# Performance work log

Measured on AMD Instinct MI355X. Metric: run time of the kernel, lower is better.

Reference implementation:

```python
import jax, jax.numpy as jnp
import numpy as np

NEG_SLOPE = 0.01  # LeakyReLU default
STRIDE = 5        # group_length // 4
EPS = 1e-5        # RMSNorm eps


def leaky_relu(x):
    return jnp.where(x >= 0, x, NEG_SLOPE * x)


def rmsnorm(x, w):
    return x * jax.lax.rsqrt(jnp.mean(x * x, axis=-1, keepdims=True) + EPS) * w


def s6(x, fc1_w, fc1_b, fc2_w, fc2_b, fc3_w, fc3_b, A):
    # x: [B, L, D] with D = 2*d_model; A: [D, N]
    delta = jax.nn.softplus(x @ fc1_w.T + fc1_b)        # [B, L, D]
    Bm = x @ fc2_w.T + fc2_b                             # [B, L, N]
    Cm = x @ fc3_w.T + fc3_b                             # [B, L, N]
    dA = jnp.exp(jnp.einsum('bld,dn->bldn', delta, A))   # [B, L, D, N]
    dBx = jnp.einsum('bld,bln,bld->bldn', delta, Bm, x)  # delta * B * x

    def step(h, inp):
        dA_t, dBx_t = inp
        h = dA_t * h + dBx_t
        return h, h

    B_, L, D, N = dA.shape
    h0 = jnp.zeros((B_, D, N), dtype=x.dtype)
    _, hs = jax.lax.scan(step, h0, (jnp.swapaxes(dA, 0, 1), jnp.swapaxes(dBx, 0, 1)))
    hs = jnp.swapaxes(hs, 0, 1)                          # [B, L, D, N]
    return jnp.einsum('bln,bldn->bld', Cm, hs)           # [B, L, D]


def setup_inputs() -> dict:
    key = jax.random.key(0)
    ks = iter(jax.random.split(key, 32))

    def rn(shape, scale=0.02):
        return scale * jax.random.normal(next(ks), shape, dtype=jnp.float32)

    B, band, gl, d, N, L = 256, 189, 20, 128, 128, 34
    di = 2 * d
    return {
        'x': jax.random.normal(next(ks), (B, 1, band), dtype=jnp.float32),
        'conv_w': rn((d, 1, gl)), 'conv_b': rn((d,)),
        'norm_w': jnp.ones((d,), jnp.float32),
        'inp_w': rn((di, d)), 'inp_b': rn((di,)),
        'seqconv_w': rn((L, L, 3)), 'seqconv_b': rn((L,)),
        'convlin_w': rn((di, di)), 'convlin_b': rn((di,)),
        'fc1_w': rn((di, di)), 'fc1_b': rn((di,)),
        'fc2_w': rn((N, di)), 'fc2_b': rn((N,)),
        'fc3_w': rn((N, di)), 'fc3_b': rn((N,)),
        'A': jnp.ones((di, N), jnp.float32) / jnp.sqrt(jnp.float32(N)),
        'D_w': rn((di, d)), 'D_b': rn((di,)),
        'out_w': rn((d, di)), 'out_b': rn((d,)),
        'fnn1_w': rn((64, L * d)), 'fnn1_b': rn((64,)),
        'fnn2_w': rn((32, 64)), 'fnn2_b': rn((32,)),
    }


def reference(x, conv_w, conv_b, norm_w, inp_w, inp_b, seqconv_w, seqconv_b,
              convlin_w, convlin_b, fc1_w, fc1_b, fc2_w, fc2_b, fc3_w, fc3_b,
              A, D_w, D_b, out_w, out_b, fnn1_w, fnn1_b, fnn2_w, fnn2_b):
    # group division: Conv1d(1, d, k=20, stride=5) + LeakyReLU
    g = jax.lax.conv_general_dilated(x, conv_w, (STRIDE,), [(0, 0)],
                                     dimension_numbers=('NCH', 'OIH', 'NCH'))
    g = leaky_relu(g + conv_b[None, :, None])            # [B, d, L]
    h = jnp.swapaxes(g, 1, 2)                            # [B, L, d]
    # Mamba block
    xn = rmsnorm(h, norm_w)
    xp = xn @ inp_w.T + inp_b                            # [B, L, 2d]
    # Conv1d(seq_len, seq_len, k=3, pad=1): seq axis L is the channel dim
    xc = jax.lax.conv_general_dilated(xp, seqconv_w, (1,), [(1, 1)],
                                      dimension_numbers=('NCH', 'OIH', 'NCH'))
    xc = jax.nn.silu(xc + seqconv_b[None, :, None])
    xc = xc @ convlin_w.T + convlin_b                    # [B, L, 2d]
    xs = s6(xc, fc1_w, fc1_b, fc2_w, fc2_b, fc3_w, fc3_b, A)
    y = jax.nn.silu(xs) * jax.nn.silu(xn @ D_w.T + D_b)  # gated
    y = y @ out_w.T + out_b                              # [B, L, d]
    # FNN head
    f = y.reshape(y.shape[0], -1)                        # [B, L*d]
    f = leaky_relu(f @ fnn1_w.T + fnn1_b)
    return f @ fnn2_w.T + fnn2_b                         # [B, 32]
```

## Files before the change

kernel.cpp:

```cpp
#include <hip/hip_runtime.h>
#include <math.h>


#define NB    256
#define LL    34
#define DD    128
#define DI    256
#define NN    128
#define MM    (NB*LL)

using u16 = unsigned short;
typedef __attribute__((ext_vector_type(8))) short short8;
typedef __attribute__((ext_vector_type(4))) float f32x4;

__device__ __forceinline__ float silu_f(float x)  { return x / (1.f + __expf(-x)); }
__device__ __forceinline__ float softplus_f(float x) {
    return fmaxf(x, 0.f) + __logf(1.f + __expf(-fabsf(x)));
}
__device__ __forceinline__ float leaky_f(float x) { return (x >= 0.f) ? x : 0.01f * x; }

__device__ __forceinline__ u16 f2bf(float x) {
    unsigned u = __float_as_uint(x);
    return (u16)((u + 0x7FFF + ((u >> 16) & 1)) >> 16);
}
__device__ __forceinline__ float bf2f(u16 h) {
    return __uint_as_float(((unsigned)h) << 16);
}
__device__ __forceinline__ void f2pair(float v, u16* h, u16* l) {
    u16 hh = f2bf(v);
    *h = hh;
    *l = f2bf(v - bf2f(hh));
}

__global__ __launch_bounds__(256)
void prep_all_k(const float* __restrict__ inp_w, const float* __restrict__ D_w,
                const float* __restrict__ fc1_w, const float* __restrict__ fc2_w,
                const float* __restrict__ fc3_w, const float* __restrict__ convlin_w,
                const float* __restrict__ out_w,
                const float* __restrict__ inp_b, const float* __restrict__ D_b,
                const float* __restrict__ fc1_b, const float* __restrict__ fc2_b,
                const float* __restrict__ fc3_b,
                const float* __restrict__ W1, const float* __restrict__ A,
                u16* __restrict__ wc1h, u16* __restrict__ wc1l,
                u16* __restrict__ wc3h, u16* __restrict__ wc3l,
                u16* __restrict__ cvh,  u16* __restrict__ cvl,
                u16* __restrict__ owh,  u16* __restrict__ owl,
                float* __restrict__ bias1, float* __restrict__ bias3,
                float* __restrict__ W1T, int* __restrict__ flag)
{
    const int bx  = blockIdx.x;
    const int tid = threadIdx.x;
    __shared__ float tile[64][65];

    if (bx < 1152) {
        int i = bx * 256 + tid;
        if (i < 65536) {
            float v = (i < 32768) ? inp_w[i] : D_w[i - 32768];
            f2pair(v, &wc1h[i], &wc1l[i]);
        } else if (i < 196608) {
            int j = i - 65536;
            float v = (j < 65536) ? fc1_w[j] : (j < 98304 ? fc2_w[j - 65536] : fc3_w[j - 98304]);
            f2pair(v, &wc3h[j], &wc3l[j]);
        } else if (i < 262144) {
            int j = i - 196608;
            f2pair(convlin_w[j], &cvh[j], &cvl[j]);
        } else if (i < 294912) {
            int j = i - 262144;
            f2pair(out_w[j], &owh[j], &owl[j]);
        }
        if (i < 512)  bias1[i] = (i < 256) ? inp_b[i] : D_b[i - 256];
        else if (i < 1024) {
            int j = i - 512;
            bias3[j] = (j < 256) ? fc1_b[j] : (j < 384 ? fc2_b[j - 256] : fc3_b[j - 384]);
        }
    } else if (bx < 1220) {
        const int bt = bx - 1152;
        for (int p = 0; p < 16; p++) {
            int idx = tid + p * 256;
            int r = idx >> 6, c = idx & 63;
            tile[r][c] = W1[(size_t)r * 4352 + bt * 64 + c];
        }
        __syncthreads();
        for (int p = 0; p < 16; p++) {
            int idx = tid + p * 256;
            int cc = idx >> 6, rr = idx & 63;
            W1T[(size_t)(bt * 64 + cc) * 64 + rr] = tile[rr][cc];
        }
    } else {
        __shared__ int s;
        if (tid == 0) s = 1;
        __syncthreads();
        bool ok = true;
        for (int k = 0; k < 128; k++) {
            int idx = tid + k * 256;
            ok &= (A[idx] == A[idx & ~127]);
        }
        if (!ok) s = 0;
        __syncthreads();
        if (tid == 0) *flag = s;
    }
}

__global__ __launch_bounds__(128)
void conv_norm_k(const float* __restrict__ x, const float* __restrict__ cw,
                 const float* __restrict__ cb, const float* __restrict__ nw,
                 u16* __restrict__ XNh, u16* __restrict__ XNl)
{
    int bl = blockIdx.x;
    int b = bl / LL, l = bl % LL;
    int c = threadIdx.x;
    const float* xr = x + (size_t)b * 189 + l * 5;
    float g = cb[c];
    #pragma unroll
    for (int k = 0; k < 20; k++) g = fmaf(xr[k], cw[c * 20 + k], g);
    g = leaky_f(g);

    float s = g * g;
    #pragma unroll
    for (int m = 32; m >= 1; m >>= 1) s += __shfl_xor(s, m);
    __shared__ float wsum[2];
    if ((threadIdx.x & 63) == 0) wsum[threadIdx.x >> 6] = s;
    __syncthreads();
    float mean = (wsum[0] + wsum[1]) * (1.f / 128.f);
    float inv = 1.f / sqrtf(mean + 1e-5f);
    float v = g * inv * nw[c];
    f2pair(v, &XNh[(size_t)bl * DD + c], &XNl[(size_t)bl * DD + c]);
}

template <int K, int EPI>
__global__ __launch_bounds__(256)
void mgemm_k(const u16* __restrict__ Ah, const u16* __restrict__ Al,
             const u16* __restrict__ Wh, const u16* __restrict__ Wl,
             const float* __restrict__ bias,
             float* __restrict__ Y, int ldy,
             u16* __restrict__ Yh, u16* __restrict__ Yl,
             u16* __restrict__ BC)
{
    const int tid  = threadIdx.x;
    const int r0   = blockIdx.x * 128;
    const int c0   = blockIdx.y * 64;
    const int wave = tid >> 6;
    const int lane = tid & 63;
    const int wm   = wave & 1;
    const int wn   = wave >> 1;
    const int l15  = lane & 15;
    const int lq   = lane >> 4;

    __shared__ u16 sAh[128][40];
    __shared__ u16 sAl[128][40];
    __shared__ u16 sBh[64][40];
    __shared__ u16 sBl[64][40];

    f32x4 acc[4][2];
    #pragma unroll
    for (int i = 0; i < 4; i++)
        #pragma unroll
        for (int j = 0; j < 2; j++) acc[i][j] = (f32x4){0.f, 0.f, 0.f, 0.f};

    const int a_row = tid >> 1;
    const int a_kb  = (tid & 1) * 16;
    const int b_row = tid >> 2;
    const int b_ko  = (tid & 3) * 8;

    for (int k0 = 0; k0 < K; k0 += 32) {
        const u16* ga = Ah + (size_t)(r0 + a_row) * K + k0 + a_kb;
        const u16* gl = Al + (size_t)(r0 + a_row) * K + k0 + a_kb;
        short8 vh0 = *(const short8*)(ga);
        short8 vh1 = *(const short8*)(ga + 8);
        short8 vl0 = *(const short8*)(gl);
        short8 vl1 = *(const short8*)(gl + 8);
        const u16* gb = Wh + (size_t)(c0 + b_row) * K + k0 + b_ko;
        const u16* gc = Wl + (size_t)(c0 + b_row) * K + k0 + b_ko;
        short8 wb = *(const short8*)(gb);
        short8 wc = *(const short8*)(gc);

        *(short8*)&sAh[a_row][a_kb]     = vh0;
        *(short8*)&sAh[a_row][a_kb + 8] = vh1;
        *(short8*)&sAl[a_row][a_kb]     = vl0;
        *(short8*)&sAl[a_row][a_kb + 8] = vl1;
        *(short8*)&sBh[b_row][b_ko] = wb;
        *(short8*)&sBl[b_row][b_ko] = wc;
        __syncthreads();

        short8 fah[4], fal[4], fbh[2], fbl[2];
        #pragma unroll
        for (int i = 0; i < 4; i++) {
            fah[i] = *(const short8*)&sAh[wm * 64 + i * 16 + l15][lq * 8];
            fal[i] = *(const short8*)&sAl[wm * 64 + i * 16 + l15][lq * 8];
        }
        #pragma unroll
        for (int j = 0; j < 2; j++) {
            fbh[j] = *(const short8*)&sBh[wn * 32 + j * 16 + l15][lq * 8];
            fbl[j] = *(const short8*)&sBl[wn * 32 + j * 16 + l15][lq * 8];
        }
        #pragma unroll
        for (int i = 0; i < 4; i++)
            #pragma unroll
            for (int j = 0; j < 2; j++) {
                acc[i][j] = __builtin_amdgcn_mfma_f32_16x16x32_bf16(fah[i], fbh[j], acc[i][j], 0, 0, 0);
                acc[i][j] = __builtin_amdgcn_mfma_f32_16x16x32_bf16(fah[i], fbl[j], acc[i][j], 0, 0, 0);
                acc[i][j] = __builtin_amdgcn_mfma_f32_16x16x32_bf16(fal[i], fbh[j], acc[i][j], 0, 0, 0);
            }
        __syncthreads();
    }

    #pragma unroll
    for (int i = 0; i < 4; i++) {
        int gr = r0 + wm * 64 + i * 16 + lq * 4;
        #pragma unroll
        for (int j = 0; j < 2; j++) {
            int gc = c0 + wn * 32 + j * 16 + l15;
            float bb = bias[gc];
            #pragma unroll
            for (int r = 0; r < 4; r++) {
                float v = acc[i][j][r] + bb;
                if (EPI == 1 || EPI == 3) { if (gc < 256) v = softplus_f(v); }
                if (EPI == 2) {
                    u16 hh, ll;
                    f2pair(v, &hh, &ll);
                    Yh[(size_t)(gr + r) * ldy + gc] = hh;
                    Yl[(size_t)(gr + r) * ldy + gc] = ll;
                } else {
                    Y[(size_t)(gr + r) * ldy + gc] = v;
                    if (EPI == 3 && gc >= 256) {
                        u16 hh, ll;
                        f2pair(v, &hh, &ll);
                        u16* rb = BC + (size_t)(gr + r) * 1024
                                     + ((gc < 384) ? 0 : 256) + (gc & 127);
                        rb[0]   = hh;
                        rb[128] = ll;
                    }
                }
            }
        }
    }
}

__global__ __launch_bounds__(256)
void seqconv_k(const float* __restrict__ XP, int ldxp,
               const float* __restrict__ w, const float* __restrict__ bias,
               u16* __restrict__ XCh, u16* __restrict__ XCl)
{
    const int b   = blockIdx.x;
    const int tid = threadIdx.x;
    const int tx  = tid & 63;
    const int ty  = tid >> 6;
    const int j0  = tx * 4;

    __shared__ float sx[LL][264];
    __shared__ float sw[LL][112];

    for (int idx = tid; idx < LL * 256; idx += 256) {
        int li = idx >> 8, jj = idx & 255;
        sx[li][jj + 1] = XP[(size_t)(b * LL + li) * ldxp + jj];
    }
    if (tid < LL) { sx[tid][0] = 0.f; sx[tid][257] = 0.f; }
    for (int idx = tid; idx < LL * LL * 3; idx += 256) {
        int lo = idx / 102;
        int rem = idx - lo * 102;
        int li = rem / 3;
        int k  = rem - li * 3;
        sw[li][lo * 3 + k] = w[idx];
    }
    __syncthreads();

    const int base = ty * 9 - (ty == 3 ? 1 : 0);
    const int cnt  = (ty < 2) ? 9 : 8;

    float acc[9][4];
    #pragma unroll
    for (int i = 0; i < 9; i++)
        #pragma unroll
        for (int jj = 0; jj < 4; jj++) acc[i][jj] = 0.f;

    for (int li = 0; li < LL; li++) {
        float4 xa = *(const float4*)&sx[li][j0];
        float2 xb = *(const float2*)&sx[li][j0 + 4];
        float xv[6] = {xa.x, xa.y, xa.z, xa.w, xb.x, xb.y};
        const float* swr = &sw[li][0];
        #pragma unroll
        for (int i = 0; i < 9; i++) {
            if (i < cnt) {
                int lo3 = (base + i) * 3;
                float w0 = swr[lo3 + 0];
                float w1 = swr[lo3 + 1];
                float w2 = swr[lo3 + 2];
                #pragma unroll
                for (int jj = 0; jj < 4; jj++) {
                    acc[i][jj] = fmaf(w0, xv[jj],     acc[i][jj]);
                    acc[i][jj] = fmaf(w1, xv[jj + 1], acc[i][jj]);
                    acc[i][jj] = fmaf(w2, xv[jj + 2], acc[i][jj]);
                }
            }
        }
    }

    #pragma unroll
    for (int i = 0; i < 9; i++) {
        if (i < cnt) {
            int lo = base + i;
            float bb = bias[lo];
            ushort4 oh, ol;
            float v0 = silu_f(acc[i][0] + bb);
            float v1 = silu_f(acc[i][1] + bb);
            float v2 = silu_f(acc[i][2] + bb);
            float v3 = silu_f(acc[i][3] + bb);
            f2pair(v0, &oh.x, &ol.x);
            f2pair(v1, &oh.y, &ol.y);
            f2pair(v2, &oh.z, &ol.z);
            f2pair(v3, &oh.w, &ol.w);
            size_t o = (size_t)(b * LL + lo) * DI + j0;
            *(ushort4*)&XCh[o] = oh;
            *(ushort4*)&XCl[o] = ol;
        }
    }
}

__global__ __launch_bounds__(256)
void ssd_scan_k(const int* __restrict__ flag,
                const float* __restrict__ dBC,
                const u16* __restrict__ BC,
                const u16* __restrict__ Xh, const u16* __restrict__ Xl,
                const float* __restrict__ A,
                const float* __restrict__ DG,
                u16* __restrict__ Gh, u16* __restrict__ Gl)
{
    if (*flag == 0) return;
    const int b    = blockIdx.x;
    const int tid  = threadIdx.x;
    const int wave = tid >> 6;
    const int lane = tid & 63;
    const int l15  = lane & 15;
    const int lq   = lane >> 4;

    __shared__ u16 sBh[48][136], sBl[48][136];
    __shared__ u16 sCh[48][136], sCl[48][136];
    __shared__ float sM[48][49];

    const u16* base = BC + (size_t)b * LL * 1024;
    for (int idx = tid; idx < LL * 16; idx += 256) {
        int l = idx >> 4, c = (idx & 15) << 3;
        const u16* row = base + l * 1024;
        *(short8*)&sBh[l][c] = *(const short8*)&row[c];
        *(short8*)&sBl[l][c] = *(const short8*)&row[128 + c];
        *(short8*)&sCh[l][c] = *(const short8*)&row[256 + c];
        *(short8*)&sCl[l][c] = *(const short8*)&row[384 + c];
    }
    __syncthreads();

    for (int tt = wave; tt < 9; tt += 4) {
        int ti = tt / 3, tj = tt - ti * 3;
        f32x4 acc = (f32x4){0.f, 0.f, 0.f, 0.f};
        #pragma unroll
        for (int ks = 0; ks < 4; ks++) {
            short8 ch = *(const short8*)&sCh[ti * 16 + l15][ks * 32 + lq * 8];
            short8 cl = *(const short8*)&sCl[ti * 16 + l15][ks * 32 + lq * 8];
            short8 bh = *(const short8*)&sBh[tj * 16 + l15][ks * 32 + lq * 8];
            short8 bl = *(const short8*)&sBl[tj * 16 + l15][ks * 32 + lq * 8];
            acc = __builtin_amdgcn_mfma_f32_16x16x32_bf16(ch, bh, acc, 0, 0, 0);
            acc = __builtin_amdgcn_mfma_f32_16x16x32_bf16(ch, bl, acc, 0, 0, 0);
            acc = __builtin_amdgcn_mfma_f32_16x16x32_bf16(cl, bh, acc, 0, 0, 0);
        }
        #pragma unroll
        for (int r = 0; r < 4; r++)
            sM[ti * 16 + lq * 4 + r][tj * 16 + l15] = acc[r];
    }
    __syncthreads();

    const int d = tid;
    const float a_d = A[(size_t)d * NN];
    const float* pDel = dBC + (size_t)b * LL * 512 + d;
    const u16* pXh = Xh + (size_t)b * LL * 256 + d;
    const u16* pXl = Xl + (size_t)b * LL * 256 + d;

    float u[LL], eS[LL];
    float S = 0.f;
    #pragma unroll
    for (int l = 0; l < LL; l++) {
        float dl = pDel[l * 512];
        S = fmaf(dl, a_d, S);
        eS[l] = __expf(S);
        float xv = bf2f(pXh[l * 256]) + bf2f(pXl[l * 256]);
        u[l] = __expf(-S) * dl * xv;
    }

    const float* pG = DG + (size_t)b * LL * 512 + 256 + d;
    u16* pGh = Gh + (size_t)b * LL * 256 + d;
    u16* pGl = Gl + (size_t)b * LL * 256 + d;
    #pragma unroll
    for (int l = 0; l < LL; l++) {
        float acc = 0.f;
        for (int t = 0; t <= l; t++) acc = fmaf(sM[l][t], u[t], acc);
        float xs = eS[l] * acc;
        float g = silu_f(xs) * silu_f(pG[l * 512]);
        u16 hh, ll2;
        f2pair(g, &hh, &ll2);
        pGh[l * 256] = hh;
        pGl[l * 256] = ll2;
    }
}

__global__ __launch_bounds__(256)
void scan_fb_k(const int* __restrict__ flag,
               const float* __restrict__ dBC,
               const u16*  __restrict__ Xh, const u16* __restrict__ Xl,
               const float* __restrict__ A,
               const float* __restrict__ DG,
               u16* __restrict__ Gh, u16* __restrict__ Gl)
{
    if (*flag != 0) return;
    const int b  = blockIdx.y;
    const int d0 = blockIdx.x * 64;
    const int tid = threadIdx.x;
    const int sub = tid & 15;
    const int pg  = tid >> 4;
    const int dbase = d0 + pg * 4;
    const int nA = sub * 4;

    float a[4][8], h[4][8];
    #pragma unroll
    for (int dd = 0; dd < 4; dd++) {
        const float* Ar = A + (size_t)(dbase + dd) * NN;
        float4 q0 = *(const float4*)(Ar + nA);
        float4 q1 = *(const float4*)(Ar + 64 + nA);
        a[dd][0]=q0.x; a[dd][1]=q0.y; a[dd][2]=q0.z; a[dd][3]=q0.w;
        a[dd][4]=q1.x; a[dd][5]=q1.y; a[dd][6]=q1.z; a[dd][7]=q1.w;
        #pragma unroll
        for (int j = 0; j < 8; j++) h[dd][j] = 0.f;
    }

    const float* pD  = dBC + (size_t)b * LL * 512 + dbase;
    const float* pBC = dBC + (size_t)b * LL * 512 + 256 + nA;
    const u16*  pXh = Xh  + (size_t)b * LL * 256 + dbase;
    const u16*  pXl = Xl  + (size_t)b * LL * 256 + dbase;
    const float* pG  = DG  + (size_t)b * LL * 512 + 256 + dbase;
    u16* pGh = Gh + (size_t)b * LL * 256 + dbase;
    u16* pGl = Gl + (size_t)b * LL * 256 + dbase;

    for (int l = 0; l < LL; l++) {
        float4  cD  = *(const float4*)(pD);
        ushort4 cXh = *(const ushort4*)(pXh);
        ushort4 cXl = *(const ushort4*)(pXl);
        float4 cB0 = *(const float4*)(pBC);
        float4 cB1 = *(const float4*)(pBC + 64);
        float4 cC0 = *(const float4*)(pBC + 128);
        float4 cC1 = *(const float4*)(pBC + 192);
        pD += 512; pBC += 512; pXh += 256; pXl += 256;

        float xv[4] = { bf2f(cXh.x) + bf2f(cXl.x), bf2f(cXh.y) + bf2f(cXl.y),
                        bf2f(cXh.z) + bf2f(cXl.z), bf2f(cXh.w) + bf2f(cXl.w) };
        float dl[4] = {cD.x, cD.y, cD.z, cD.w};
        float dx[4] = {cD.x * xv[0], cD.y * xv[1], cD.z * xv[2], cD.w * xv[3]};
        float bv[8] = {cB0.x,cB0.y,cB0.z,cB0.w,cB1.x,cB1.y,cB1.z,cB1.w};
        float cv[8] = {cC0.x,cC0.y,cC0.z,cC0.w,cC1.x,cC1.y,cC1.z,cC1.w};

        float accd[4] = {0.f, 0.f, 0.f, 0.f};
        #pragma unroll
        for (int dd = 0; dd < 4; dd++)
            #pragma unroll
            for (int j = 0; j < 8; j++) {
                float dA = __expf(dl[dd] * a[dd][j]);
                h[dd][j] = fmaf(dA, h[dd][j], dx[dd] * bv[j]);
                accd[dd] = fmaf(cv[j], h[dd][j], accd[dd]);
            }
        #pragma unroll
        for (int dd = 0; dd < 4; dd++) {
            float v = accd[dd];
            v += __shfl_xor(v, 1);
            v += __shfl_xor(v, 2);
            v += __shfl_xor(v, 4);
            v += __shfl_xor(v, 8);
            accd[dd] = v;
        }
        if (sub == 0) {
            float4 dg = *(const float4*)(pG);
            ushort4 oh, ol;
            float g0 = silu_f(accd[0]) * silu_f(dg.x);
            float g1 = silu_f(accd[1]) * silu_f(dg.y);
            float g2 = silu_f(accd[2]) * silu_f(dg.z);
            float g3 = silu_f(accd[3]) * silu_f(dg.w);
            f2pair(g0, &oh.x, &ol.x);
            f2pair(g1, &oh.y, &ol.y);
            f2pair(g2, &oh.z, &ol.z);
            f2pair(g3, &oh.w, &ol.w);
            *(ushort4*)pGh = oh;
            *(ushort4*)pGl = ol;
        }
        pG += 512; pGh += 256; pGl += 256;
    }
}

__global__ __launch_bounds__(256)
void fnn1_k(const float* __restrict__ F, const float* __restrict__ W1T,
            float* __restrict__ partials)
{
    const int btile = blockIdx.x;
    const int kc    = blockIdx.y;
    const int tid   = threadIdx.x;
    __shared__ float sf[16][260];
    for (int i = tid; i < 16 * 256; i += 256) {
        int r = i >> 8, c = i & 255;
        sf[r][c] = F[(size_t)(btile * 16 + r) * 4352 + kc * 256 + c];
    }
    __syncthreads();

    const int o  = tid & 63;
    const int bq = tid >> 6;
    const float* w = W1T + (size_t)(kc * 256) * 64 + o;
    float acc[4] = {0.f, 0.f, 0.f, 0.f};
    for (int k = 0; k < 256; k += 4) {
        float w0 = w[(size_t)(k + 0) * 64];
        float w1 = w[(size_t)(k + 1) * 64];
        float w2 = w[(size_t)(k + 2) * 64];
        float w3 = w[(size_t)(k + 3) * 64];
        #pragma unroll
        for (int bj = 0; bj < 4; bj++) {
            float4 f4 = *(const float4*)&sf[bq * 4 + bj][k];
            acc[bj] = fmaf(w0, f4.x, acc[bj]);
            acc[bj] = fmaf(w1, f4.y, acc[bj]);
            acc[bj] = fmaf(w2, f4.z, acc[bj]);
            acc[bj] = fmaf(w3, f4.w, acc[bj]);
        }
    }
    #pragma unroll
    for (int bj = 0; bj < 4; bj++)
        partials[(size_t)kc * 16384 + (btile * 16 + bq * 4 + bj) * 64 + o] = acc[bj];
}

__global__ __launch_bounds__(64)
void fnn2_k(const float* __restrict__ partials,
            const float* __restrict__ B1,
            const float* __restrict__ W2, const float* __restrict__ B2,
            float* __restrict__ out)
{
    int b = blockIdx.x;
    int t = threadIdx.x;
    __shared__ float s1[64];
    float acc = B1[t];
    #pragma unroll
    for (int kc = 0; kc < 17; kc++)
        acc += partials[(size_t)kc * 16384 + b * 64 + t];
    s1[t] = leaky_f(acc);
    __syncthreads();

    if (t < 32) {
        float acc2 = B2[t];
        const float* w2 = W2 + t * 64;
        #pragma unroll
        for (int j = 0; j < 64; j++) acc2 = fmaf(s1[j], w2[j], acc2);
        out[(size_t)b * 32 + t] = acc2;
    }
}

extern "C" void kernel_launch(void* const* d_in, const int* in_sizes, int n_in,
                              void* d_out, int out_size, void* d_ws, size_t ws_size,
                              hipStream_t stream)
{
    const float* x        = (const float*)d_in[0];
    const float* conv_w   = (const float*)d_in[1];
    const float* conv_b   = (const float*)d_in[2];
    const float* norm_w   = (const float*)d_in[3];
    const float* inp_w    = (const float*)d_in[4];
    const float* inp_b    = (const float*)d_in[5];
    const float* seqconv_w= (const float*)d_in[6];
    const float* seqconv_b= (const float*)d_in[7];
    const float* convlin_w= (const float*)d_in[8];
    const float* convlin_b= (const float*)d_in[9];
    const float* fc1_w    = (const float*)d_in[10];
    const float* fc1_b    = (const float*)d_in[11];
    const float* fc2_w    = (const float*)d_in[12];
    const float* fc2_b    = (const float*)d_in[13];
    const float* fc3_w    = (const float*)d_in[14];
    const float* fc3_b    = (const float*)d_in[15];
    const float* A        = (const float*)d_in[16];
    const float* D_w      = (const float*)d_in[17];
    const float* D_b      = (const float*)d_in[18];
    const float* out_w    = (const float*)d_in[19];
    const float* out_b    = (const float*)d_in[20];
    const float* fnn1_w   = (const float*)d_in[21];
    const float* fnn1_b   = (const float*)d_in[22];
    const float* fnn2_w   = (const float*)d_in[23];
    const float* fnn2_b   = (const float*)d_in[24];

    char* W = (char*)d_ws;
    float* buf1  = (float*)(W + 0);
    float* buf3  = (float*)(W + 17825792);
    u16*   xnh   = (u16*)  (W + 35651584);
    u16*   xnl   = (u16*)  (W + 37879808);
    u16*   xc2h  = (u16*)  (W + 35651584);
    float* fout  = (float*)(W + 35651584);
    u16*   xc2l  = (u16*)  (W + 40108032);
    u16*   xch   = (u16*)  (W + 44564480);
    u16*   xcl   = (u16*)  (W + 49020928);
    float* w1t   = (float*)(W + 53477376);
    u16*   wc1h  = (u16*)  (W + 54591488);
    u16*   wc1l  = (u16*)  (W + 54722560);
    u16*   wc3h  = (u16*)  (W + 54853632);
    u16*   wc3l  = (u16*)  (W + 55115776);
    u16*   cvh   = (u16*)  (W + 55377920);
    u16*   cvl   = (u16*)  (W + 55508992);
    u16*   owh   = (u16*)  (W + 55640064);
    u16*   owl   = (u16*)  (W + 55705600);
    float* bias1 = (float*)(W + 55771136);
    float* bias3 = (float*)(W + 55773184);
    int*   uflag = (int*)  (W + 55775232);
    u16* gateh = xch;
    u16* gatel = xcl;
    u16* bcpair = (u16*)buf1;
    float* partials = buf3;

    prep_all_k<<<1221, 256, 0, stream>>>(inp_w, D_w, fc1_w, fc2_w, fc3_w,
                                         convlin_w, out_w,
                                         inp_b, D_b, fc1_b, fc2_b, fc3_b,
                                         fnn1_w, A,
                                         wc1h, wc1l, wc3h, wc3l, cvh, cvl,
                                         owh, owl, bias1, bias3, w1t, uflag);

    conv_norm_k<<<MM, 128, 0, stream>>>(x, conv_w, conv_b, norm_w, xnh, xnl);

    mgemm_k<128, 0><<<dim3(MM / 128, 8), 256, 0, stream>>>(
        xnh, xnl, wc1h, wc1l, bias1, buf1, 512, nullptr, nullptr, nullptr);

    seqconv_k<<<NB, 256, 0, stream>>>(buf1, 512, seqconv_w, seqconv_b, xch, xcl);

    mgemm_k<256, 2><<<dim3(MM / 128, 4), 256, 0, stream>>>(
        xch, xcl, cvh, cvl, convlin_b, nullptr, 256, xc2h, xc2l, nullptr);

    mgemm_k<256, 3><<<dim3(MM / 128, 8), 256, 0, stream>>>(
        xc2h, xc2l, wc3h, wc3l, bias3, buf3, 512, nullptr, nullptr, bcpair);

    ssd_scan_k<<<NB, 256, 0, stream>>>(uflag, buf3, bcpair, xc2h, xc2l, A,
                                       buf1, gateh, gatel);
    scan_fb_k<<<dim3(4, NB), 256, 0, stream>>>(uflag, buf3, xc2h, xc2l, A,
                                               buf1, gateh, gatel);

    mgemm_k<256, 0><<<dim3(MM / 128, 2), 256, 0, stream>>>(
        gateh, gatel, owh, owl, out_b, fout, 128, nullptr, nullptr, nullptr);

    fnn1_k<<<dim3(16, 17), 256, 0, stream>>>(fout, w1t, partials);
    fnn2_k<<<NB, 64, 0, stream>>>(partials, fnn1_b, fnn2_w, fnn2_b,
                                  (float*)d_out);
}
```

Measured before the change: 220.5 us.

## Fuse conv, norm, GEMMs, seqconv, scan and out-proj into one per-batch kernel

Replaces the chain of separate kernels (conv+norm, input GEMM, seq conv, convlin GEMM, fc GEMM, scan, out GEMM) with one kernel that runs one workgroup per batch element. Intermediates stay in shared memory and registers rather than going through global memory. GEMMs read weight fragments directly from global memory without LDS staging. The risk is low parallelism: only 256 workgroups of 256 threads with launch_bounds(256,1) and heavy register use, so each CU runs one block serially through every stage.

```diff
diff --git a/kernel.cpp b/kernel.cpp
--- a/kernel.cpp
+++ b/kernel.cpp
@@ -51,6 +51,7 @@
     const int bx  = blockIdx.x;
     const int tid = threadIdx.x;
     __shared__ float tile[64][65];
+    __shared__ int sflag;
 
     if (bx < 1152) {
         int i = bx * 256 + tid;
@@ -87,245 +88,63 @@
             W1T[(size_t)(bt * 64 + cc) * 64 + rr] = tile[rr][cc];
         }
     } else {
-        __shared__ int s;
-        if (tid == 0) s = 1;
+        if (tid == 0) sflag = 1;
         __syncthreads();
         bool ok = true;
         for (int k = 0; k < 128; k++) {
             int idx = tid + k * 256;
             ok &= (A[idx] == A[idx & ~127]);
         }
-        if (!ok) s = 0;
-        __syncthreads();
-        if (tid == 0) *flag = s;
-    }
-}
-
-__global__ __launch_bounds__(128)
-void conv_norm_k(const float* __restrict__ x, const float* __restrict__ cw,
-                 const float* __restrict__ cb, const float* __restrict__ nw,
-                 u16* __restrict__ XNh, u16* __restrict__ XNl)
+        if (!ok) sflag = 0;
+        __syncthreads();
+        if (tid == 0) *flag = sflag;
+    }
+}
+
+template <int KS, int NT>
+__device__ __forceinline__ void gemm3t(
+    const u16* __restrict__ Ah, const u16* __restrict__ Al, int astr,
+    const u16* __restrict__ Wh, const u16* __restrict__ Wl, int K,
+    int colbase, int l15, int lq, f32x4 (&acc)[3][NT])
 {
-    int bl = blockIdx.x;
-    int b = bl / LL, l = bl % LL;
-    int c = threadIdx.x;
-    const float* xr = x + (size_t)b * 189 + l * 5;
-    float g = cb[c];
-    #pragma unroll
-    for (int k = 0; k < 20; k++) g = fmaf(xr[k], cw[c * 20 + k], g);
-    g = leaky_f(g);
-
-    float s = g * g;
-    #pragma unroll
-    for (int m = 32; m >= 1; m >>= 1) s += __shfl_xor(s, m);
-    __shared__ float wsum[2];
-    if ((threadIdx.x & 63) == 0) wsum[threadIdx.x >> 6] = s;
-    __syncthreads();
-    float mean = (wsum[0] + wsum[1]) * (1.f / 128.f);
-    float inv = 1.f / sqrtf(mean + 1e-5f);
-    float v = g * inv * nw[c];
-    f2pair(v, &XNh[(size_t)bl * DD + c], &XNl[(size_t)bl * DD + c]);
-}
-
-template <int K, int EPI>
-__global__ __launch_bounds__(256)
-void mgemm_k(const u16* __restrict__ Ah, const u16* __restrict__ Al,
-             const u16* __restrict__ Wh, const u16* __restrict__ Wl,
-             const float* __restrict__ bias,
-             float* __restrict__ Y, int ldy,
-             u16* __restrict__ Yh, u16* __restrict__ Yl,
-             u16* __restrict__ BC)
+    for (int ks = 0; ks < KS; ks++) {
+        short8 fah[3], fal[3];
+        #pragma unroll
+        for (int ti = 0; ti < 3; ti++) {
+            fah[ti] = *(const short8*)&Ah[(ti * 16 + l15) * astr + ks * 32 + lq * 8];
+            fal[ti] = *(const short8*)&Al[(ti * 16 + l15) * astr + ks * 32 + lq * 8];
+        }
+        #pragma unroll
+        for (int nt = 0; nt < NT; nt++) {
+            size_t off = (size_t)(colbase + nt * 16 + l15) * K + ks * 32 + lq * 8;
+            short8 bh = *(const short8*)&Wh[off];
+            short8 bl = *(const short8*)&Wl[off];
+            #pragma unroll
+            for (int ti = 0; ti < 3; ti++) {
+                acc[ti][nt] = __builtin_amdgcn_mfma_f32_16x16x32_bf16(fah[ti], bh, acc[ti][nt], 0, 0, 0);
+                acc[ti][nt] = __builtin_amdgcn_mfma_f32_16x16x32_bf16(fah[ti], bl, acc[ti][nt], 0, 0, 0);
+                acc[ti][nt] = __builtin_amdgcn_mfma_f32_16x16x32_bf16(fal[ti], bh, acc[ti][nt], 0, 0, 0);
+            }
+        }
+    }
+}
+
+__global__ __launch_bounds__(256, 1)
+void fused_k(const float* __restrict__ xin, const float* __restrict__ cw,
+             const float* __restrict__ cb, const float* __restrict__ nw,
+             const u16* __restrict__ wc1h, const u16* __restrict__ wc1l,
+             const float* __restrict__ bias1,
+             const float* __restrict__ scw, const float* __restrict__ scb,
+             const u16* __restrict__ cvh, const u16* __restrict__ cvl,
+             const float* __restrict__ cvb,
+             const u16* __restrict__ wc3h, const u16* __restrict__ wc3l,
+             const float* __restrict__ bias3,
+             const float* __restrict__ A, const int* __restrict__ flag,
+             const u16* __restrict__ owh, const u16* __restrict__ owl,
+             const float* __restrict__ owb,
+             float* __restrict__ dg_g, float* __restrict__ delta_g,
+             u16* __restrict__ bc_g, float* __restrict__ fout_g)
 {
-    const int tid  = threadIdx.x;
-    const int r0   = blockIdx.x * 128;
-    const int c0   = blockIdx.y * 64;
-    const int wave = tid >> 6;
-    const int lane = tid & 63;
-    const int wm   = wave & 1;
-    const int wn   = wave >> 1;
-    const int l15  = lane & 15;
-    const int lq   = lane >> 4;
-
-    __shared__ u16 sAh[128][40];
-    __shared__ u16 sAl[128][40];
-    __shared__ u16 sBh[64][40];
-    __shared__ u16 sBl[64][40];
-
-    f32x4 acc[4][2];
-    #pragma unroll
-    for (int i = 0; i < 4; i++)
-        #pragma unroll
-        for (int j = 0; j < 2; j++) acc[i][j] = (f32x4){0.f, 0.f, 0.f, 0.f};
-
-    const int a_row = tid >> 1;
-    const int a_kb  = (tid & 1) * 16;
-    const int b_row = tid >> 2;
-    const int b_ko  = (tid & 3) * 8;
-
-    for (int k0 = 0; k0 < K; k0 += 32) {
-        const u16* ga = Ah + (size_t)(r0 + a_row) * K + k0 + a_kb;
-        const u16* gl = Al + (size_t)(r0 + a_row) * K + k0 + a_kb;
-        short8 vh0 = *(const short8*)(ga);
-        short8 vh1 = *(const short8*)(ga + 8);
-        short8 vl0 = *(const short8*)(gl);
-        short8 vl1 = *(const short8*)(gl + 8);
-        const u16* gb = Wh + (size_t)(c0 + b_row) * K + k0 + b_ko;
-        const u16* gc = Wl + (size_t)(c0 + b_row) * K + k0 + b_ko;
-        short8 wb = *(const short8*)(gb);
-        short8 wc = *(const short8*)(gc);
-
-        *(short8*)&sAh[a_row][a_kb]     = vh0;
-        *(short8*)&sAh[a_row][a_kb + 8] = vh1;
-        *(short8*)&sAl[a_row][a_kb]     = vl0;
-        *(short8*)&sAl[a_row][a_kb + 8] = vl1;
-        *(short8*)&sBh[b_row][b_ko] = wb;
-        *(short8*)&sBl[b_row][b_ko] = wc;
-        __syncthreads();
-
-        short8 fah[4], fal[4], fbh[2], fbl[2];
-        #pragma unroll
-        for (int i = 0; i < 4; i++) {
-            fah[i] = *(const short8*)&sAh[wm * 64 + i * 16 + l15][lq * 8];
-            fal[i] = *(const short8*)&sAl[wm * 64 + i * 16 + l15][lq * 8];
-        }
-        #pragma unroll
-        for (int j = 0; j < 2; j++) {
-            fbh[j] = *(const short8*)&sBh[wn * 32 + j * 16 + l15][lq * 8];
-            fbl[j] = *(const short8*)&sBl[wn * 32 + j * 16 + l15][lq * 8];
-        }
-        #pragma unroll
-        for (int i = 0; i < 4; i++)
-            #pragma unroll
-            for (int j = 0; j < 2; j++) {
-                acc[i][j] = __builtin_amdgcn_mfma_f32_16x16x32_bf16(fah[i], fbh[j], acc[i][j], 0, 0, 0);
-                acc[i][j] = __builtin_amdgcn_mfma_f32_16x16x32_bf16(fah[i], fbl[j], acc[i][j], 0, 0, 0);
-                acc[i][j] = __builtin_amdgcn_mfma_f32_16x16x32_bf16(fal[i], fbh[j], acc[i][j], 0, 0, 0);
-            }
-        __syncthreads();
-    }
-
-    #pragma unroll
-    for (int i = 0; i < 4; i++) {
-        int gr = r0 + wm * 64 + i * 16 + lq * 4;
-        #pragma unroll
-        for (int j = 0; j < 2; j++) {
-            int gc = c0 + wn * 32 + j * 16 + l15;
-            float bb = bias[gc];
-            #pragma unroll
-            for (int r = 0; r < 4; r++) {
-                float v = acc[i][j][r] + bb;
-                if (EPI == 1 || EPI == 3) { if (gc < 256) v = softplus_f(v); }
-                if (EPI == 2) {
-                    u16 hh, ll;
-                    f2pair(v, &hh, &ll);
-                    Yh[(size_t)(gr + r) * ldy + gc] = hh;
-                    Yl[(size_t)(gr + r) * ldy + gc] = ll;
-                } else {
-                    Y[(size_t)(gr + r) * ldy + gc] = v;
-                    if (EPI == 3 && gc >= 256) {
-                        u16 hh, ll;
-                        f2pair(v, &hh, &ll);
-                        u16* rb = BC + (size_t)(gr + r) * 1024
-                                     + ((gc < 384) ? 0 : 256) + (gc & 127);
-                        rb[0]   = hh;
-                        rb[128] = ll;
-                    }
-                }
-            }
-        }
-    }
-}
-
-__global__ __launch_bounds__(256)
-void seqconv_k(const float* __restrict__ XP, int ldxp,
-               const float* __restrict__ w, const float* __restrict__ bias,
-               u16* __restrict__ XCh, u16* __restrict__ XCl)
-{
-    const int b   = blockIdx.x;
-    const int tid = threadIdx.x;
-    const int tx  = tid & 63;
-    const int ty  = tid >> 6;
-    const int j0  = tx * 4;
-
-    __shared__ float sx[LL][264];
-    __shared__ float sw[LL][112];
-
-    for (int idx = tid; idx < LL * 256; idx += 256) {
-        int li = idx >> 8, jj = idx & 255;
-        sx[li][jj + 1] = XP[(size_t)(b * LL + li) * ldxp + jj];
-    }
-    if (tid < LL) { sx[tid][0] = 0.f; sx[tid][257] = 0.f; }
-    for (int idx = tid; idx < LL * LL * 3; idx += 256) {
-        int lo = idx / 102;
-        int rem = idx - lo * 102;
-        int li = rem / 3;
-        int k  = rem - li * 3;
-        sw[li][lo * 3 + k] = w[idx];
-    }
-    __syncthreads();
-
-    const int base = ty * 9 - (ty == 3 ? 1 : 0);
-    const int cnt  = (ty < 2) ? 9 : 8;
-
-    float acc[9][4];
-    #pragma unroll
-    for (int i = 0; i < 9; i++)
-        #pragma unroll
-        for (int jj = 0; jj < 4; jj++) acc[i][jj] = 0.f;
-
-    for (int li = 0; li < LL; li++) {
-        float4 xa = *(const float4*)&sx[li][j0];
-        float2 xb = *(const float2*)&sx[li][j0 + 4];
-        float xv[6] = {xa.x, xa.y, xa.z, xa.w, xb.x, xb.y};
-        const float* swr = &sw[li][0];
-        #pragma unroll
-        for (int i = 0; i < 9; i++) {
-            if (i < cnt) {
-                int lo3 = (base + i) * 3;
-                float w0 = swr[lo3 + 0];
-                float w1 = swr[lo3 + 1];
-                float w2 = swr[lo3 + 2];
-                #pragma unroll
-                for (int jj = 0; jj < 4; jj++) {
-                    acc[i][jj] = fmaf(w0, xv[jj],     acc[i][jj]);
-                    acc[i][jj] = fmaf(w1, xv[jj + 1], acc[i][jj]);
-                    acc[i][jj] = fmaf(w2, xv[jj + 2], acc[i][jj]);
-                }
-            }
-        }
-    }
-
-    #pragma unroll
-    for (int i = 0; i < 9; i++) {
-        if (i < cnt) {
-            int lo = base + i;
-            float bb = bias[lo];
-            ushort4 oh, ol;
-            float v0 = silu_f(acc[i][0] + bb);
-            float v1 = silu_f(acc[i][1] + bb);
-            float v2 = silu_f(acc[i][2] + bb);
-            float v3 = silu_f(acc[i][3] + bb);
-            f2pair(v0, &oh.x, &ol.x);
-            f2pair(v1, &oh.y, &ol.y);
-            f2pair(v2, &oh.z, &ol.z);
-            f2pair(v3, &oh.w, &ol.w);
-            size_t o = (size_t)(b * LL + lo) * DI + j0;
-            *(ushort4*)&XCh[o] = oh;
-            *(ushort4*)&XCl[o] = ol;
-        }
-    }
-}
-
-__global__ __launch_bounds__(256)
-void ssd_scan_k(const int* __restrict__ flag,
-                const float* __restrict__ dBC,
-                const u16* __restrict__ BC,
-                const u16* __restrict__ Xh, const u16* __restrict__ Xl,
-                const float* __restrict__ A,
-                const float* __restrict__ DG,
-                u16* __restrict__ Gh, u16* __restrict__ Gl)
-{
-    if (*flag == 0) return;
     const int b    = blockIdx.x;
     const int tid  = threadIdx.x;
     const int wave = tid >> 6;
@@ -333,160 +152,284 @@
     const int l15  = lane & 15;
     const int lq   = lane >> 4;
 
-    __shared__ u16 sBh[48][136], sBl[48][136];
-    __shared__ u16 sCh[48][136], sCl[48][136];
-    __shared__ float sM[48][49];
-
-    const u16* base = BC + (size_t)b * LL * 1024;
+    __shared__ __align__(16) char pool[62464];
+    u16*   XNh   = (u16*)(pool);
+    u16*   XNl   = (u16*)(pool + 9248);
+    float* R1f   = (float*)(pool + 18496);
+    u16*   R1h   = (u16*)(pool + 18496);
+    u16*   R1l   = (u16*)(pool + 36448);
+    float* sxrow = (float*)(pool + 18496);
+    float* spart = (float*)(pool + 19328);
+    float* sw    = (float*)(pool);
+    u16*   sBh   = (u16*)(pool);
+    u16*   sBl   = (u16*)(pool + 9248);
+    u16*   sCh   = (u16*)(pool + 18496);
+    u16*   sCl   = (u16*)(pool + 27744);
+    float* sM    = (float*)(pool + 36992);
+    u16*   Gth   = (u16*)(pool);
+    u16*   Gtl   = (u16*)(pool + 17952);
+
+    if (tid < 192) sxrow[tid] = (tid < 189) ? xin[(size_t)b * 189 + tid] : 0.f;
+    __syncthreads();
+    for (int p = 0; p < 17; p++) {
+        int idx = p * 256 + tid;
+        int l = idx >> 7, c = idx & 127;
+        float g = cb[c];
+        #pragma unroll
+        for (int k = 0; k < 20; k++) g = fmaf(sxrow[l * 5 + k], cw[c * 20 + k], g);
+        g = leaky_f(g);
+        f2pair(g, &XNh[l * 136 + c], &XNl[l * 136 + c]);
+        float s = g * g;
+        #pragma unroll
+        for (int m = 32; m >= 1; m >>= 1) s += __shfl_xor(s, m);
+        if (lane == 0) spart[l * 2 + ((tid >> 6) & 1)] = s;
+        __syncthreads();
+    }
+    for (int p = 0; p < 17; p++) {
+        int idx = p * 256 + tid;
+        int l = idx >> 7, c = idx & 127;
+        float mean = (spart[l * 2] + spart[l * 2 + 1]) * (1.f / 128.f);
+        float inv = 1.f / sqrtf(mean + 1e-5f);
+        float g = bf2f(XNh[l * 136 + c]) + bf2f(XNl[l * 136 + c]);
+        float v = g * inv * nw[c];
+        f2pair(v, &XNh[l * 136 + c], &XNl[l * 136 + c]);
+    }
+    __syncthreads();
+
+    {
+        f32x4 a1[3][8];
+        #pragma unroll
+        for (int i = 0; i < 3; i++)
+            #pragma unroll
+            for (int j = 0; j < 8; j++) a1[i][j] = (f32x4){0.f, 0.f, 0.f, 0.f};
+        gemm3t<4, 8>(XNh, XNl, 136, wc1h, wc1l, 128, wave * 128, l15, lq, a1);
+        __syncthreads();
+        #pragma unroll
+        for (int ti = 0; ti < 3; ti++) {
+            #pragma unroll
+            for (int nt = 0; nt < 8; nt++) {
+                int gc = wave * 128 + nt * 16 + l15;
+                float bb = bias1[gc];
+                #pragma unroll
+                for (int r = 0; r < 4; r++) {
+                    int gr = ti * 16 + lq * 4 + r;
+                    if (gr < 34) {
+                        float v = a1[ti][nt][r] + bb;
+                        if (gc < 256) R1f[gr * 264 + gc] = v;
+                        else dg_g[(size_t)(b * 34 + gr) * 256 + (gc - 256)] = v;
+                    }
+                }
+            }
+        }
+    }
+    for (int idx = tid; idx < LL * LL * 3; idx += 256) {
+        int lo = idx / 102;
+        int rem = idx - lo * 102;
+        int li = rem / 3;
+        int k  = rem - li * 3;
+        sw[li * 104 + lo * 3 + k] = scw[idx];
+    }
+    __syncthreads();
+
+    {
+        const int j = tid;
+        float acc[34];
+        #pragma unroll
+        for (int lo = 0; lo < 34; lo++) acc[lo] = 0.f;
+        for (int li = 0; li < 34; li++) {
+            float x0  = R1f[li * 264 + j];
+            float xm  = (j > 0)   ? R1f[li * 264 + j - 1] : 0.f;
+            float xp1 = (j < 255) ? R1f[li * 264 + j + 1] : 0.f;
+            const float* wr = &sw[li * 104];
+            #pragma unroll
+            for (int lo = 0; lo < 34; lo++) {
+                acc[lo] = fmaf(wr[lo * 3 + 0], xm,  acc[lo]);
+                acc[lo] = fmaf(wr[lo * 3 + 1], x0,  acc[lo]);
+                acc[lo] = fmaf(wr[lo * 3 + 2], xp1, acc[lo]);
+            }
+        }
+        __syncthreads();
+        #pragma unroll
+        for (int lo = 0; lo < 34; lo++) {
+            float v = silu_f(acc[lo] + scb[lo]);
+            f2pair(v, &R1h[lo * 264 + j], &R1l[lo * 264 + j]);
+        }
+        __syncthreads();
+    }
+
+    {
+        f32x4 a2[3][4];
+        #pragma unroll
+        for (int i = 0; i < 3; i++)
+            #pragma unroll
+            for (int j = 0; j < 4; j++) a2[i][j] = (f32x4){0.f, 0.f, 0.f, 0.f};
+        gemm3t<8, 4>(R1h, R1l, 264, cvh, cvl, 256, wave * 64, l15, lq, a2);
+        __syncthreads();
+        #pragma unroll
+        for (int ti = 0; ti < 3; ti++) {
+            #pragma unroll
+            for (int nt = 0; nt < 4; nt++) {
+                int gc = wave * 64 + nt * 16 + l15;
+                float bb = cvb[gc];
+                #pragma unroll
+                for (int r = 0; r < 4; r++) {
+                    int gr = ti * 16 + lq * 4 + r;
+                    if (gr < 34) {
+                        float v = a2[ti][nt][r] + bb;
+                        f2pair(v, &R1h[gr * 264 + gc], &R1l[gr * 264 + gc]);
+                    }
+                }
+            }
+        }
+        __syncthreads();
+    }
+
+    float xreg[34];
+    #pragma unroll
+    for (int l = 0; l < 34; l++)
+        xreg[l] = bf2f(R1h[l * 264 + tid]) + bf2f(R1l[l * 264 + tid]);
+
+    {
+        f32x4 a3[3][8];
+        #pragma unroll
+        for (int i = 0; i < 3; i++)
+            #pragma unroll
+            for (int j = 0; j < 8; j++) a3[i][j] = (f32x4){0.f, 0.f, 0.f, 0.f};
+        gemm3t<8, 8>(R1h, R1l, 264, wc3h, wc3l, 256, wave * 128, l15, lq, a3);
+        #pragma unroll
+        for (int ti = 0; ti < 3; ti++) {
+            #pragma unroll
+            for (int nt = 0; nt < 8; nt++) {
+                int gc = wave * 128 + nt * 16 + l15;
+                float bb = bias3[gc];
+                #pragma unroll
+                for (int r = 0; r < 4; r++) {
+                    int gr = ti * 16 + lq * 4 + r;
+                    if (gr < 34) {
+                        float v = a3[ti][nt][r] + bb;
+                        if (gc < 256) {
+                            delta_g[(size_t)(b * 34 + gr) * 256 + gc] = softplus_f(v);
+                        } else {
+                            u16 hh, ll;
+                            f2pair(v, &hh, &ll);
+                            u16* rb = bc_g + (size_t)(b * 34 + gr) * 1024
+                                           + ((gc < 384) ? 0 : 256) + (gc & 127);
+                            rb[0]   = hh;
+                            rb[128] = ll;
+                        }
+                    }
+                }
+            }
+        }
+        __syncthreads();
+    }
+
     for (int idx = tid; idx < LL * 16; idx += 256) {
         int l = idx >> 4, c = (idx & 15) << 3;
-        const u16* row = base + l * 1024;
-        *(short8*)&sBh[l][c] = *(const short8*)&row[c];
-        *(short8*)&sBl[l][c] = *(const short8*)&row[128 + c];
-        *(short8*)&sCh[l][c] = *(const short8*)&row[256 + c];
-        *(short8*)&sCl[l][c] = *(const short8*)&row[384 + c];
-    }
-    __syncthreads();
-
-    for (int tt = wave; tt < 9; tt += 4) {
-        int ti = tt / 3, tj = tt - ti * 3;
-        f32x4 acc = (f32x4){0.f, 0.f, 0.f, 0.f};
-        #pragma unroll
-        for (int ks = 0; ks < 4; ks++) {
-            short8 ch = *(const short8*)&sCh[ti * 16 + l15][ks * 32 + lq * 8];
-            short8 cl = *(const short8*)&sCl[ti * 16 + l15][ks * 32 + lq * 8];
-            short8 bh = *(const short8*)&sBh[tj * 16 + l15][ks * 32 + lq * 8];
-            short8 bl = *(const short8*)&sBl[tj * 16 + l15][ks * 32 + lq * 8];
-            acc = __builtin_amdgcn_mfma_f32_16x16x32_bf16(ch, bh, acc, 0, 0, 0);
-            acc = __builtin_amdgcn_mfma_f32_16x16x32_bf16(ch, bl, acc, 0, 0, 0);
-            acc = __builtin_amdgcn_mfma_f32_16x16x32_bf16(cl, bh, acc, 0, 0, 0);
-        }
-        #pragma unroll
-        for (int r = 0; r < 4; r++)
-            sM[ti * 16 + lq * 4 + r][tj * 16 + l15] = acc[r];
-    }
-    __syncthreads();
-
+        const u16* row = bc_g + (size_t)(b * 34 + l) * 1024;
+        *(short8*)&sBh[l * 136 + c] = *(const short8*)&row[c];
+        *(short8*)&sBl[l * 136 + c] = *(const short8*)&row[128 + c];
+        *(short8*)&sCh[l * 136 + c] = *(const short8*)&row[256 + c];
+        *(short8*)&sCl[l * 136 + c] = *(const short8*)&row[384 + c];
+    }
+    __syncthreads();
+
+    const int uni = *flag;
     const int d = tid;
-    const float a_d = A[(size_t)d * NN];
-    const float* pDel = dBC + (size_t)b * LL * 512 + d;
-    const u16* pXh = Xh + (size_t)b * LL * 256 + d;
-    const u16* pXl = Xl + (size_t)b * LL * 256 + d;
-
-    float u[LL], eS[LL];
-    float S = 0.f;
-    #pragma unroll
-    for (int l = 0; l < LL; l++) {
-        float dl = pDel[l * 512];
-        S = fmaf(dl, a_d, S);
-        eS[l] = __expf(S);
-        float xv = bf2f(pXh[l * 256]) + bf2f(pXl[l * 256]);
-        u[l] = __expf(-S) * dl * xv;
-    }
-
-    const float* pG = DG + (size_t)b * LL * 512 + 256 + d;
-    u16* pGh = Gh + (size_t)b * LL * 256 + d;
-    u16* pGl = Gl + (size_t)b * LL * 256 + d;
-    #pragma unroll
-    for (int l = 0; l < LL; l++) {
-        float acc = 0.f;
-        for (int t = 0; t <= l; t++) acc = fmaf(sM[l][t], u[t], acc);
-        float xs = eS[l] * acc;
-        float g = silu_f(xs) * silu_f(pG[l * 512]);
-        u16 hh, ll2;
-        f2pair(g, &hh, &ll2);
-        pGh[l * 256] = hh;
-        pGl[l * 256] = ll2;
-    }
-}
-
-__global__ __launch_bounds__(256)
-void scan_fb_k(const int* __restrict__ flag,
-               const float* __restrict__ dBC,
-               const u16*  __restrict__ Xh, const u16* __restrict__ Xl,
-               const float* __restrict__ A,
-               const float* __restrict__ DG,
-               u16* __restrict__ Gh, u16* __restrict__ Gl)
-{
-    if (*flag != 0) return;
-    const int b  = blockIdx.y;
-    const int d0 = blockIdx.x * 64;
-    const int tid = threadIdx.x;
-    const int sub = tid & 15;
-    const int pg  = tid >> 4;
-    const int dbase = d0 + pg * 4;
-    const int nA = sub * 4;
-
-    float a[4][8], h[4][8];
-    #pragma unroll
-    for (int dd = 0; dd < 4; dd++) {
-        const float* Ar = A + (size_t)(dbase + dd) * NN;
-        float4 q0 = *(const float4*)(Ar + nA);
-        float4 q1 = *(const float4*)(Ar + 64 + nA);
-        a[dd][0]=q0.x; a[dd][1]=q0.y; a[dd][2]=q0.z; a[dd][3]=q0.w;
-        a[dd][4]=q1.x; a[dd][5]=q1.y; a[dd][6]=q1.z; a[dd][7]=q1.w;
-        #pragma unroll
-        for (int j = 0; j < 8; j++) h[dd][j] = 0.f;
-    }
-
-    const float* pD  = dBC + (size_t)b * LL * 512 + dbase;
-    const float* pBC = dBC + (size_t)b * LL * 512 + 256 + nA;
-    const u16*  pXh = Xh  + (size_t)b * LL * 256 + dbase;
-    const u16*  pXl = Xl  + (size_t)b * LL * 256 + dbase;
-    const float* pG  = DG  + (size_t)b * LL * 512 + 256 + dbase;
-    u16* pGh = Gh + (size_t)b * LL * 256 + dbase;
-    u16* pGl = Gl + (size_t)b * LL * 256 + dbase;
-
-    for (int l = 0; l < LL; l++) {
-        float4  cD  = *(const float4*)(pD);
-        ushort4 cXh = *(const ushort4*)(pXh);
-        ushort4 cXl = *(const ushort4*)(pXl);
-        float4 cB0 = *(const float4*)(pBC);
-        float4 cB1 = *(const float4*)(pBC + 64);
-        float4 cC0 = *(const float4*)(pBC + 128);
-        float4 cC1 = *(const float4*)(pBC + 192);
-        pD += 512; pBC += 512; pXh += 256; pXl += 256;
-
-        float xv[4] = { bf2f(cXh.x) + bf2f(cXl.x), bf2f(cXh.y) + bf2f(cXl.y),
-                        bf2f(cXh.z) + bf2f(cXl.z), bf2f(cXh.w) + bf2f(cXl.w) };
-        float dl[4] = {cD.x, cD.y, cD.z, cD.w};
-        float dx[4] = {cD.x * xv[0], cD.y * xv[1], cD.z * xv[2], cD.w * xv[3]};
-        float bv[8] = {cB0.x,cB0.y,cB0.z,cB0.w,cB1.x,cB1.y,cB1.z,cB1.w};
-        float cv[8] = {cC0.x,cC0.y,cC0.z,cC0.w,cC1.x,cC1.y,cC1.z,cC1.w};
-
-        float accd[4] = {0.f, 0.f, 0.f, 0.f};
-        #pragma unroll
-        for (int dd = 0; dd < 4; dd++)
-            #pragma unroll
-            for (int j = 0; j < 8; j++) {
-                float dA = __expf(dl[dd] * a[dd][j]);
-                h[dd][j] = fmaf(dA, h[dd][j], dx[dd] * bv[j]);
-                accd[dd] = fmaf(cv[j], h[dd][j], accd[dd]);
-            }
-        #pragma unroll
-        for (int dd = 0; dd < 4; dd++) {
-            float v = accd[dd];
-            v += __shfl_xor(v, 1);
-            v += __shfl_xor(v, 2);
-            v += __shfl_xor(v, 4);
-            v += __shfl_xor(v, 8);
-            accd[dd] = v;
-        }
-        if (sub == 0) {
-            float4 dg = *(const float4*)(pG);
-            ushort4 oh, ol;
-            float g0 = silu_f(accd[0]) * silu_f(dg.x);
-            float g1 = silu_f(accd[1]) * silu_f(dg.y);
-            float g2 = silu_f(accd[2]) * silu_f(dg.z);
-            float g3 = silu_f(accd[3]) * silu_f(dg.w);
-            f2pair(g0, &oh.x, &ol.x);
-            f2pair(g1, &oh.y, &ol.y);
-            f2pair(g2, &oh.z, &ol.z);
-            f2pair(g3, &oh.w, &ol.w);
-            *(ushort4*)pGh = oh;
-            *(ushort4*)pGl = ol;
-        }
-        pG += 512; pGh += 256; pGl += 256;
+
+    if (uni != 0) {
+        for (int tt = wave; tt < 9; tt += 4) {
+            int ti = tt / 3, tj = tt - ti * 3;
+            f32x4 macc = (f32x4){0.f, 0.f, 0.f, 0.f};
+            #pragma unroll
+            for (int ks = 0; ks < 4; ks++) {
+                short8 ch = *(const short8*)&sCh[(ti * 16 + l15) * 136 + ks * 32 + lq * 8];
+                short8 cl = *(const short8*)&sCl[(ti * 16 + l15) * 136 + ks * 32 + lq * 8];
+                short8 bh = *(const short8*)&sBh[(tj * 16 + l15) * 136 + ks * 32 + lq * 8];
+                short8 bl = *(const short8*)&sBl[(tj * 16 + l15) * 136 + ks * 32 + lq * 8];
+                macc = __builtin_amdgcn_mfma_f32_16x16x32_bf16(ch, bh, macc, 0, 0, 0);
+                macc = __builtin_amdgcn_mfma_f32_16x16x32_bf16(ch, bl, macc, 0, 0, 0);
+                macc = __builtin_amdgcn_mfma_f32_16x16x32_bf16(cl, bh, macc, 0, 0, 0);
+            }
+            #pragma unroll
+            for (int r = 0; r < 4; r++)
+                sM[(ti * 16 + lq * 4 + r) * 48 + tj * 16 + l15] = macc[r];
+        }
+        __syncthreads();
+
+        const float a_d = A[(size_t)d * NN];
+        float u[34], eS[34];
+        float S = 0.f;
+        #pragma unroll
+        for (int l = 0; l < 34; l++) {
+            float dl = delta_g[(size_t)(b * 34 + l) * 256 + d];
+            S = fmaf(dl, a_d, S);
+            eS[l] = __expf(S);
+            u[l] = __expf(-S) * dl * xreg[l];
+        }
+        #pragma unroll
+        for (int l = 0; l < 34; l++) {
+            float acc = 0.f;
+            #pragma unroll
+            for (int t = 0; t <= l; t++) acc = fmaf(sM[l * 48 + t], u[t], acc);
+            float xsv = eS[l] * acc;
+            float g = silu_f(xsv) * silu_f(dg_g[(size_t)(b * 34 + l) * 256 + d]);
+            f2pair(g, &Gth[l * 264 + d], &Gtl[l * 264 + d]);
+        }
+    } else {
+        const float* Arow = A + (size_t)d * NN;
+        float h[128];
+        #pragma unroll
+        for (int n = 0; n < 128; n++) h[n] = 0.f;
+        for (int l = 0; l < 34; l++) {
+            float dl = delta_g[(size_t)(b * 34 + l) * 256 + d];
+            float dx = dl * xreg[l];
+            float accp = 0.f;
+            #pragma unroll
+            for (int n = 0; n < 128; n++) {
+                float Bv = bf2f(sBh[l * 136 + n]) + bf2f(sBl[l * 136 + n]);
+                float Cv = bf2f(sCh[l * 136 + n]) + bf2f(sCl[l * 136 + n]);
+                float dA = __expf(dl * Arow[n]);
+                h[n] = fmaf(dA, h[n], dx * Bv);
+                accp = fmaf(Cv, h[n], accp);
+            }
+            float g = silu_f(accp) * silu_f(dg_g[(size_t)(b * 34 + l) * 256 + d]);
+            u16 hh, ll;
+            f2pair(g, &hh, &ll);
+            u16* rb = bc_g + (size_t)(b * 34 + l) * 1024 + d;
+            rb[0]   = hh;
+            rb[512] = ll;
+        }
+        __syncthreads();
+        for (int l = 0; l < 34; l++) {
+            const u16* rb = bc_g + (size_t)(b * 34 + l) * 1024 + d;
+            Gth[l * 264 + d] = rb[0];
+            Gtl[l * 264 + d] = rb[512];
+        }
+    }
+    __syncthreads();
+
+    {
+        f32x4 a4[3][2];
+        #pragma unroll
+        for (int i = 0; i < 3; i++)
+            #pragma unroll
+            for (int j = 0; j < 2; j++) a4[i][j] = (f32x4){0.f, 0.f, 0.f, 0.f};
+        gemm3t<8, 2>(Gth, Gtl, 264, owh, owl, 256, wave * 32, l15, lq, a4);
+        #pragma unroll
+        for (int ti = 0; ti < 3; ti++) {
+            #pragma unroll
+            for (int nt = 0; nt < 2; nt++) {
+                int gc = wave * 32 + nt * 16 + l15;
+                float bb = owb[gc];
+                #pragma unroll
+                for (int r = 0; r < 4; r++) {
+                    int gr = ti * 16 + lq * 4 + r;
+                    if (gr < 34)
+                        fout_g[(size_t)(b * 34 + gr) * 128 + gc] = a4[ti][nt][r] + bb;
+                }
+            }
+        }
     }
 }
 
@@ -583,31 +526,23 @@
     const float* fnn2_b   = (const float*)d_in[24];
 
     char* W = (char*)d_ws;
-    float* buf1  = (float*)(W + 0);
-    float* buf3  = (float*)(W + 17825792);
-    u16*   xnh   = (u16*)  (W + 35651584);
-    u16*   xnl   = (u16*)  (W + 37879808);
-    u16*   xc2h  = (u16*)  (W + 35651584);
-    float* fout  = (float*)(W + 35651584);
-    u16*   xc2l  = (u16*)  (W + 40108032);
-    u16*   xch   = (u16*)  (W + 44564480);
-    u16*   xcl   = (u16*)  (W + 49020928);
-    float* w1t   = (float*)(W + 53477376);
-    u16*   wc1h  = (u16*)  (W + 54591488);
-    u16*   wc1l  = (u16*)  (W + 54722560);
-    u16*   wc3h  = (u16*)  (W + 54853632);
-    u16*   wc3l  = (u16*)  (W + 55115776);
-    u16*   cvh   = (u16*)  (W + 55377920);
-    u16*   cvl   = (u16*)  (W + 55508992);
-    u16*   owh   = (u16*)  (W + 55640064);
-    u16*   owl   = (u16*)  (W + 55705600);
-    float* bias1 = (float*)(W + 55771136);
-    float* bias3 = (float*)(W + 55773184);
-    int*   uflag = (int*)  (W + 55775232);
-    u16* gateh = xch;
-    u16* gatel = xcl;
-    u16* bcpair = (u16*)buf1;
-    float* partials = buf3;
+    float* dg_g    = (float*)(W + 0);
+    float* delta_g = (float*)(W + 8912896);
+    u16*   bc_g    = (u16*)  (W + 17825792);
+    float* fout_g  = (float*)(W + 35651584);
+    float* w1t     = (float*)(W + 40108032);
+    float* partials= (float*)(W + 41222144);
+    u16*   wc1h    = (u16*)  (W + 42336256);
+    u16*   wc1l    = (u16*)  (W + 42467328);
+    u16*   wc3h    = (u16*)  (W + 42598400);
+    u16*   wc3l    = (u16*)  (W + 42860544);
+    u16*   cvh     = (u16*)  (W + 43122688);
+    u16*   cvl     = (u16*)  (W + 43253760);
+    u16*   owh     = (u16*)  (W + 43384832);
+    u16*   owl     = (u16*)  (W + 43450368);
+    float* bias1   = (float*)(W + 43515904);
+    float* bias3   = (float*)(W + 43517952);
+    int*   uflag   = (int*)  (W + 43520000);
 
     prep_all_k<<<1221, 256, 0, stream>>>(inp_w, D_w, fc1_w, fc2_w, fc3_w,
                                          convlin_w, out_w,
@@ -616,28 +551,16 @@
                                          wc1h, wc1l, wc3h, wc3l, cvh, cvl,
                                          owh, owl, bias1, bias3, w1t, uflag);
 
-    conv_norm_k<<<MM, 128, 0, stream>>>(x, conv_w, conv_b, norm_w, xnh, xnl);
-
-    mgemm_k<128, 0><<<dim3(MM / 128, 8), 256, 0, stream>>>(
-        xnh, xnl, wc1h, wc1l, bias1, buf1, 512, nullptr, nullptr, nullptr);
-
-    seqconv_k<<<NB, 256, 0, stream>>>(buf1, 512, seqconv_w, seqconv_b, xch, xcl);
-
-    mgemm_k<256, 2><<<dim3(MM / 128, 4), 256, 0, stream>>>(
-        xch, xcl, cvh, cvl, convlin_b, nullptr, 256, xc2h, xc2l, nullptr);
-
-    mgemm_k<256, 3><<<dim3(MM / 128, 8), 256, 0, stream>>>(
-        xc2h, xc2l, wc3h, wc3l, bias3, buf3, 512, nullptr, nullptr, bcpair);
-
-    ssd_scan_k<<<NB, 256, 0, stream>>>(uflag, buf3, bcpair, xc2h, xc2l, A,
-                                       buf1, gateh, gatel);
-    scan_fb_k<<<dim3(4, NB), 256, 0, stream>>>(uflag, buf3, xc2h, xc2l, A,
-                                               buf1, gateh, gatel);
-
-    mgemm_k<256, 0><<<dim3(MM / 128, 2), 256, 0, stream>>>(
-        gateh, gatel, owh, owl, out_b, fout, 128, nullptr, nullptr, nullptr);
-
-    fnn1_k<<<dim3(16, 17), 256, 0, stream>>>(fout, w1t, partials);
+    fused_k<<<NB, 256, 0, stream>>>(x, conv_w, conv_b, norm_w,
+                                    wc1h, wc1l, bias1,
+                                    seqconv_w, seqconv_b,
+                                    cvh, cvl, convlin_b,
+                                    wc3h, wc3l, bias3,
+                                    A, uflag,
+                                    owh, owl, out_b,
+                                    dg_g, delta_g, bc_g, fout_g);
+
+    fnn1_k<<<dim3(16, 17), 256, 0, stream>>>(fout_g, w1t, partials);
     fnn2_k<<<NB, 64, 0, stream>>>(partials, fnn1_b, fnn2_w, fnn2_b,
                                   (float*)d_out);
 }
```

Result: slower. 228.2 us (+3.5%).
